# Kernel optimization log

Measured on AMD Instinct MI355X. Metric: run time of the kernel, lower is better.

## Reference

```python
import jax, jax.numpy as jnp
import numpy as np

ACT_DIM = 768
DICT_SIZE = 32768
S0 = 4096          # top-level latent size (dict_size // prod(lower sizes))
S1 = 8             # lower_level_latent_sizes[0]
K = 64             # per-token top-k (applied globally as k * batch)


def setup_inputs() -> dict:
    key = jax.random.key(0)
    ks = jax.random.split(key, 7)
    scale_e = 1.0 / np.sqrt(ACT_DIM)
    scale_d = 1.0 / np.sqrt(DICT_SIZE)
    return {
        "x": jax.random.normal(ks[0], (4096, ACT_DIM), dtype=jnp.float32),
        "W0": jax.random.normal(ks[1], (S0, ACT_DIM), dtype=jnp.float32) * scale_e,
        "b0": jnp.zeros((S0,), dtype=jnp.float32),
        "W1": jax.random.normal(ks[2], (DICT_SIZE, ACT_DIM), dtype=jnp.float32) * scale_e,
        "b1": jnp.zeros((DICT_SIZE,), dtype=jnp.float32),
        "Wd": jax.random.normal(ks[3], (ACT_DIM, DICT_SIZE), dtype=jnp.float32) * scale_d,
        "b_dec": jnp.zeros((ACT_DIM,), dtype=jnp.float32),
    }


def reference(x, W0, b0, W1, b1, Wd, b_dec):
    B = x.shape[0]
    x_centered = x - b_dec                                   # [B, D]
    # hierarchical relu encoders
    l0 = jax.nn.relu(x_centered @ W0.T + b0)                 # [B, S0]
    l1 = jax.nn.relu(x_centered @ W1.T + b1)                 # [B, S0*S1]
    # multiplicative gating: lower-level gate broadcast over finest level
    final_dense = (l1.reshape(B, S0, S1) * l0[:, :, None]).reshape(B, S0 * S1)
    # global batch top-k over flattened [B * dict_size]
    flat = final_dense.reshape(-1)
    k_for_batch = min(K * B, flat.shape[0])
    vals, idx = jax.lax.top_k(flat, k_for_batch)
    sparse_flat = jnp.zeros_like(flat).at[idx].set(vals)
    encoded = sparse_flat.reshape(B, S0 * S1)
    # decode
    x_hat = encoded @ Wd.T + b_dec                           # [B, D]
    return x_hat
```

## Files before the change

### kernel.cpp

```cpp
#include <hip/hip_runtime.h>
#include <stdint.h>

#define DDIM 768
#define BROWS 4096
#define S0N 4096
#define DICT 32768
#define KTOT 262144u
#define PREF 2.0f
#define DELTA 4e-3f
#define CAND_CAP 8388608u
#define BAND_CAP 4096

static constexpr size_t OFF_XH   = 0;
static constexpr size_t OFF_XL   = 6291456;
static constexpr size_t OFF_W0H  = 12582912;
static constexpr size_t OFF_W0L  = 18874368;
static constexpr size_t OFF_W1H  = 25165824;
static constexpr size_t OFF_W1L  = 75497472;
static constexpr size_t OFF_WDT  = 0;
static constexpr size_t OFF_CTRL = 192937984;
static constexpr size_t OFF_ROWC = 193069056;
static constexpr size_t OFF_ROWD = 193085440;
static constexpr size_t OFF_CAND = 201474048;
static constexpr size_t WS_NEED  = 268582912;


typedef __attribute__((ext_vector_type(8))) short bf16x8;
typedef __attribute__((ext_vector_type(4))) float f32x4;

__device__ __forceinline__ unsigned umin_(unsigned a, unsigned b) { return a < b ? a : b; }
__device__ __forceinline__ float relu_(float v) { return v > 0.f ? v : 0.f; }

__device__ __forceinline__ unsigned short f2bf(float f) {
    union { float f; unsigned u; } v; v.f = f;
    unsigned r = v.u + 0x7FFFu + ((v.u >> 16) & 1u);
    return (unsigned short)(r >> 16);
}
__device__ __forceinline__ float bf2f(unsigned short h) {
    union { float f; unsigned u; } v; v.u = ((unsigned)h) << 16;
    return v.f;
}
__device__ __forceinline__ void split1(float a, short& h, short& l) {
    unsigned short hb = f2bf(a);
    float rem = a - bf2f(hb);
    h = (short)hb;
    l = (short)f2bf(rem);
}

__device__ __forceinline__ void gl16(const void* g, void* l) {
    __builtin_amdgcn_global_load_lds(
        (const __attribute__((address_space(1))) void*)g,
        (__attribute__((address_space(3))) void*)l,
        16, 0, 0);
}

__global__ void k_split_x(const float* __restrict__ x, const float* __restrict__ b_dec,
                          short* __restrict__ XH, short* __restrict__ XL) {
    int i = blockIdx.x * 256 + threadIdx.x;
    float4 xv = ((const float4*)x)[i];
    int d = (i % (DDIM / 4)) * 4;
    float4 bv = *(const float4*)(b_dec + d);
    float a[4] = {xv.x - bv.x, xv.y - bv.y, xv.z - bv.z, xv.w - bv.w};
    short4 h, lo;
    split1(a[0], h.x, lo.x); split1(a[1], h.y, lo.y);
    split1(a[2], h.z, lo.z); split1(a[3], h.w, lo.w);
    ((short4*)XH)[i] = h;
    ((short4*)XL)[i] = lo;
}

__global__ void k_split_w(const float* __restrict__ W, short* __restrict__ H,
                          short* __restrict__ L) {
    int i = blockIdx.x * 256 + threadIdx.x;
    float4 wv = ((const float4*)W)[i];
    short4 h, lo;
    split1(wv.x, h.x, lo.x); split1(wv.y, h.y, lo.y);
    split1(wv.z, h.z, lo.z); split1(wv.w, h.w, lo.w);
    ((short4*)H)[i] = h;
    ((short4*)L)[i] = lo;
}

__global__ void k_transpose(const float* __restrict__ Wd, unsigned short* __restrict__ WdT) {
    __shared__ float tile[32][33];
    int j0 = blockIdx.x * 32, d0 = blockIdx.y * 32;
    int tx = threadIdx.x & 31, ty = threadIdx.x >> 5;
#pragma unroll
    for (int i = 0; i < 4; ++i)
        tile[ty + i * 8][tx] = Wd[(size_t)(d0 + ty + i * 8) * DICT + j0 + tx];
    __syncthreads();
#pragma unroll
    for (int i = 0; i < 4; ++i)
        WdT[(size_t)(j0 + ty + i * 8) * DDIM + d0 + tx] = f2bf(tile[tx][ty + i * 8]);
}

__launch_bounds__(512, 2) __global__
void k_mm(const short* __restrict__ XH, const short* __restrict__ XL,
          const short* __restrict__ WH, const short* __restrict__ WL,
          const short* __restrict__ GH, const short* __restrict__ GL,
          const float* __restrict__ bias1, const float* __restrict__ bias0,
          uint2* __restrict__ cand, unsigned* __restrict__ ctrl) {
    __shared__ __align__(16) char smem[139264];

    const int t = threadIdx.x;
    const int w = t >> 6, l = t & 63;
    const int wm = w >> 2, wn = w & 3;
    const int lr = l & 15, lk = l >> 4;

    const int nwg = gridDim.x;
    const int bid = blockIdx.x;
    const int swz = (bid & 7) * (nwg >> 3) + (bid >> 3);
    const int bm = (swz & 15) << 8;
    const int bn = (swz >> 4) << 8;

    const int a0 = 2 * w, a1 = a0 + 1;
    const unsigned aB0 = (unsigned)(bm + (a0 >> 3) * 128 + (a0 & 7) * 16 + lr) * 768u + (unsigned)(lk * 8);
    const unsigned aB1 = (unsigned)(bm + (a1 >> 3) * 128 + (a1 & 7) * 16 + lr) * 768u + (unsigned)(lk * 8);
    const unsigned bB0 = (unsigned)(bn + (a0 >> 2) * 64 + (a0 & 3) * 16 + lr) * 768u + (unsigned)(lk * 8);
    const unsigned bB1 = (unsigned)(bn + (a1 >> 2) * 64 + (a1 & 3) * 16 + lr) * 768u + (unsigned)(lk * 8);
    const unsigned gB0 = (unsigned)((bn >> 3) + w * 16 + lr) * 768u + (unsigned)(lk * 8);
    const int cg0 = (w >> 2) * 8 + (w & 3) * 2;

    f32x4 acc[8][4];
#pragma unroll
    for (int i = 0; i < 8; ++i)
#pragma unroll
        for (int j = 0; j < 4; ++j) acc[i][j] = (f32x4){0.f, 0.f, 0.f, 0.f};
    f32x4 acc_g[2][2];
#pragma unroll
    for (int i = 0; i < 2; ++i)
#pragma unroll
        for (int j = 0; j < 2; ++j) acc_g[i][j] = (f32x4){0.f, 0.f, 0.f, 0.f};

#pragma unroll
    for (int J = 0; J < 3; ++J) {
        const unsigned kb = (unsigned)J * 32u;
        char* dA = smem + J * 16384 + a0 * 1024;
        char* dB = smem + 65536 + J * 16384 + a0 * 1024;
        gl16(XH + aB0 + kb, dA);
        gl16(XH + aB1 + kb, dA + 1024);
        gl16(WH + bB0 + kb, dB);
        gl16(WH + bB1 + kb, dB + 1024);
        if (w < 2) gl16(GH + gB0 + kb, smem + 131072 + J * 2048 + w * 1024);
    }

#pragma unroll 1
    for (int H = 0; H < 72; ++H) {
        if (w < 2) {
            if (H < 70)       asm volatile("s_waitcnt vmcnt(10)" ::: "memory");
            else if (H == 70) asm volatile("s_waitcnt vmcnt(5)" ::: "memory");
            else              asm volatile("s_waitcnt vmcnt(0)" ::: "memory");
        } else {
            if (H < 70)       asm volatile("s_waitcnt vmcnt(8)" ::: "memory");
            else if (H == 70) asm volatile("s_waitcnt vmcnt(4)" ::: "memory");
            else              asm volatile("s_waitcnt vmcnt(0)" ::: "memory");
        }
        __builtin_amdgcn_s_barrier();

        const char* rA = smem + (H & 3) * 16384;
        const char* rB = smem + 65536 + (H & 3) * 16384;
        const char* rG = smem + 131072 + (H & 3) * 2048;

        const int J = H + 3;
        const short* As = XH; const short* Bs = WH; const short* Gs = GH; unsigned kb = 0;
        char* dA = nullptr; char* dB = nullptr; char* dG = nullptr;
        const bool hj = J < 72;
        if (hj) {
            const int ktJ = J >> 1;
            if (ktJ < 12)      { As = XH; Bs = WH; Gs = GH; kb = (unsigned)ktJ * 64u; }
            else if (ktJ < 24) { As = XH; Bs = WL; Gs = GL; kb = (unsigned)(ktJ - 12) * 64u; }
            else               { As = XL; Bs = WH; Gs = GH; kb = (unsigned)(ktJ - 24) * 64u; }
            kb += (unsigned)(J & 1) * 32u;
            dA = smem + (J & 3) * 16384 + a0 * 1024;
            dB = smem + 65536 + (J & 3) * 16384 + a0 * 1024;
            dG = smem + 131072 + (J & 3) * 2048 + w * 1024;
        }

        bf16x8 bfr[4], af[4], bg0, bg1, ag;
#pragma unroll
        for (int nj = 0; nj < 4; ++nj)
            bfr[nj] = *(const bf16x8*)(rB + (wn * 4 + nj) * 1024 + l * 16);
#pragma unroll
        for (int m2 = 0; m2 < 4; ++m2)
            af[m2] = *(const bf16x8*)(rA + (wm * 8 + m2) * 1024 + l * 16);
        bg0 = *(const bf16x8*)(rG + l * 16);
        bg1 = *(const bf16x8*)(rG + 1024 + l * 16);
        ag  = *(const bf16x8*)(rA + cg0 * 1024 + l * 16);
        if (hj) {
            gl16(As + aB0 + kb, dA); gl16(As + aB1 + kb, dA + 1024);
            if (w < 2) gl16(Gs + gB0 + kb, dG);
        }
        __builtin_amdgcn_sched_barrier(0);
        __builtin_amdgcn_s_barrier();
        asm volatile("s_waitcnt lgkmcnt(0)" ::: "memory");
        __builtin_amdgcn_sched_barrier(0);
        __builtin_amdgcn_s_setprio(1);
#pragma unroll
        for (int m2 = 0; m2 < 4; ++m2)
#pragma unroll
            for (int nj = 0; nj < 4; ++nj)
                acc[m2][nj] = __builtin_amdgcn_mfma_f32_16x16x32_bf16(
                    af[m2], bfr[nj], acc[m2][nj], 0, 0, 0);
        acc_g[0][0] = __builtin_amdgcn_mfma_f32_16x16x32_bf16(ag, bg0, acc_g[0][0], 0, 0, 0);
        acc_g[0][1] = __builtin_amdgcn_mfma_f32_16x16x32_bf16(ag, bg1, acc_g[0][1], 0, 0, 0);
        __builtin_amdgcn_s_setprio(0);
        __builtin_amdgcn_s_barrier();

#pragma unroll
        for (int m2 = 0; m2 < 4; ++m2)
            af[m2] = *(const bf16x8*)(rA + (wm * 8 + 4 + m2) * 1024 + l * 16);
        ag = *(const bf16x8*)(rA + (cg0 + 1) * 1024 + l * 16);
        if (hj) { gl16(Bs + bB0 + kb, dB); gl16(Bs + bB1 + kb, dB + 1024); }
        __builtin_amdgcn_sched_barrier(0);
        __builtin_amdgcn_s_barrier();
        asm volatile("s_waitcnt lgkmcnt(0)" ::: "memory");
        __builtin_amdgcn_sched_barrier(0);
        __builtin_amdgcn_s_setprio(1);
#pragma unroll
        for (int m2 = 0; m2 < 4; ++m2)
#pragma unroll
            for (int nj = 0; nj < 4; ++nj)
                acc[4 + m2][nj] = __builtin_amdgcn_mfma_f32_16x16x32_bf16(
                    af[m2], bfr[nj], acc[4 + m2][nj], 0, 0, 0);
        acc_g[1][0] = __builtin_amdgcn_mfma_f32_16x16x32_bf16(ag, bg0, acc_g[1][0], 0, 0, 0);
        acc_g[1][1] = __builtin_amdgcn_mfma_f32_16x16x32_bf16(ag, bg1, acc_g[1][1], 0, 0, 0);
        __builtin_amdgcn_s_setprio(0);
        __builtin_amdgcn_s_barrier();
    }
    __syncthreads();

    float*    gate  = (float*)smem;
    unsigned* pscan = (unsigned*)(smem + 36864);
    const int s0base = bn >> 3;
#pragma unroll
    for (int ri = 0; ri < 2; ++ri)
#pragma unroll
        for (int ci = 0; ci < 2; ++ci)
#pragma unroll
            for (int r = 0; r < 4; ++r) {
                const int grow = w * 32 + ri * 16 + lk * 4 + r;
                const int gcol = ci * 16 + lr;
                gate[grow * 33 + gcol] = relu_(acc_g[ri][ci][r] + bias0[s0base + gcol]);
            }
    __syncthreads();

    unsigned cnt = 0;
#pragma unroll
    for (int mi = 0; mi < 8; ++mi)
#pragma unroll
        for (int nj = 0; nj < 4; ++nj)
#pragma unroll
            for (int r = 0; r < 4; ++r) {
                const int lrow = wm * 128 + mi * 16 + lk * 4 + r;
                const int lcol = wn * 64 + nj * 16 + lr;
                float v = relu_(acc[mi][nj][r] + bias1[bn + lcol]);
                v *= gate[lrow * 33 + (lcol >> 3)];
                acc[mi][nj][r] = v;
                cnt += (v >= PREF) ? 1u : 0u;
            }
    pscan[t] = cnt;
    __syncthreads();
    for (int s = 1; s < 512; s <<= 1) {
        unsigned v2 = (t >= s) ? pscan[t - s] : 0u;
        __syncthreads();
        pscan[t] += v2;
        __syncthreads();
    }
    if (t == 511) pscan[512] = atomicAdd(&ctrl[0], pscan[511]);
    __syncthreads();
    unsigned off = pscan[512] + pscan[t] - cnt;
#pragma unroll
    for (int mi = 0; mi < 8; ++mi)
#pragma unroll
        for (int nj = 0; nj < 4; ++nj)
#pragma unroll
            for (int r = 0; r < 4; ++r) {
                const float v = acc[mi][nj][r];
                if (v >= PREF) {
                    const int row = bm + wm * 128 + mi * 16 + lk * 4 + r;
                    const int col = bn + wn * 64 + nj * 16 + lr;
                    if (off < CAND_CAP)
                        cand[off] = make_uint2(__float_as_uint(v),
                                               ((unsigned)row << 15) | (unsigned)col);
                    ++off;
                }
            }
}

__global__ void k_hist1(const uint2* __restrict__ cand, unsigned* __restrict__ ctrl) {
    __shared__ unsigned h[2048];
    for (int i = threadIdx.x; i < 2048; i += 256) h[i] = 0;
    __syncthreads();
    unsigned n = umin_(ctrl[0], CAND_CAP);
    for (unsigned i = blockIdx.x * 256 + threadIdx.x; i < n; i += gridDim.x * 256)
        atomicAdd(&h[cand[i].x >> 20], 1u);
    __syncthreads();
    unsigned* hist = ctrl + 256;
    for (int i = threadIdx.x; i < 2048; i += 256)
        if (h[i]) atomicAdd(&hist[i], h[i]);
}

__global__ void k_scan1(unsigned* __restrict__ ctrl) {
    __shared__ unsigned hs[2048];
    __shared__ unsigned cs[256];
    const unsigned* h = ctrl + 256;
    int t = threadIdx.x;
    for (int i = t; i < 2048; i += 256) hs[i] = h[i];
    __syncthreads();
    unsigned s = 0;
    for (int b = 0; b < 8; ++b) s += hs[t * 8 + b];
    cs[t] = s;
    __syncthreads();
    if (t == 0) {
        unsigned cum = 0, T = 0, cb = 0;
        for (int c = 255; c >= 0; --c) {
            if (cum + cs[c] >= KTOT) {
                for (int b = c * 8 + 7; b >= c * 8; --b) {
                    cum += hs[b];
                    if (cum >= KTOT) { T = (unsigned)b; cb = cum - hs[b]; break; }
                }
                break;
            }
            cum += cs[c];
        }
        ctrl[1] = T; ctrl[2] = cb;
    }
}

__global__ void k_hist2(const uint2* __restrict__ cand, unsigned* __restrict__ ctrl) {
    unsigned n = umin_(ctrl[0], CAND_CAP);
    unsigned T = ctrl[1];
    unsigned* hist2 = ctrl + 2304;
    for (unsigned i = blockIdx.x * 256 + threadIdx.x; i < n; i += gridDim.x * 256) {
        unsigned u = cand[i].x;
        if ((u >> 20) == T) atomicAdd(&hist2[(u >> 8) & 0xFFFu], 1u);
    }
}

__global__ void k_scan2(unsigned* __restrict__ ctrl) {
    __shared__ unsigned hs[4096];
    __shared__ unsigned cs[256];
    const unsigned* h = ctrl + 2304;
    int t = threadIdx.x;
    for (int i = t; i < 4096; i += 256) hs[i] = h[i];
    __syncthreads();
    unsigned s = 0;
    for (int b = 0; b < 16; ++b) s += hs[t * 16 + b];
    cs[t] = s;
    __syncthreads();
    if (t == 0) {
        unsigned cum = ctrl[2], T2 = 0;
        for (int c = 255; c >= 0; --c) {
            if (cum + cs[c] >= KTOT) {
                for (int b = c * 16 + 15; b >= c * 16; --b) {
                    cum += hs[b];
                    if (cum >= KTOT) { T2 = (unsigned)b; break; }
                }
                break;
            }
            cum += cs[c];
        }
        ctrl[3] = (ctrl[1] << 12) | T2;
    }
}

__global__ void k_band_rows(const uint2* __restrict__ cand, unsigned* __restrict__ ctrl,
                            unsigned* __restrict__ rowc, uint2* __restrict__ rowd) {
    __shared__ unsigned lhi;
    if (threadIdx.x == 0) lhi = 0;
    __syncthreads();
    unsigned n = umin_(ctrl[0], CAND_CAP);
    unsigned H = ctrl[3];
    float lo = __uint_as_float(H << 8) - DELTA;
    float hi = __uint_as_float((H + 1u) << 8) + DELTA;
    unsigned* band_idx = ctrl + 6400;
    unsigned my = 0;
    for (unsigned i = blockIdx.x * 256 + threadIdx.x; i < n; i += gridDim.x * 256) {
        uint2 cv = cand[i];
        float v = __uint_as_float(cv.x);
        if (v > hi) {
            ++my;
            unsigned b = cv.y >> 15;
            unsigned p = atomicAdd(&rowc[b], 1u);
            if (p < 256u) rowd[(b << 8) + p] = make_uint2(cv.y & 32767u, cv.x);
        } else if (v >= lo) {
            unsigned p = atomicAdd(&ctrl[5], 1u);
            if (p < BAND_CAP) band_idx[p] = cv.y;
        }
    }
    atomicAdd(&lhi, my);
    __syncthreads();
    if (threadIdx.x == 0 && lhi) atomicAdd(&ctrl[4], lhi);
}

__global__ void k_f64(const float* __restrict__ x, const float* __restrict__ b_dec,
                      const float* __restrict__ W0, const float* __restrict__ b0,
                      const float* __restrict__ W1, const float* __restrict__ b1,
                      const unsigned* __restrict__ ctrl, double* __restrict__ band_v) {
    unsigned n = umin_(ctrl[5], BAND_CAP);
    unsigned bi = blockIdx.x;
    if (bi >= n) return;
    const unsigned* band_idx = ctrl + 6400;
    unsigned idx = band_idx[bi];
    int b = idx >> 15, j = idx & 32767, s0 = j >> 3;
    int lane = threadIdx.x;
    const float* xr = x + (size_t)b * DDIM;
    const float* w1 = W1 + (size_t)j * DDIM;
    const float* w0 = W0 + (size_t)s0 * DDIM;
    double d1 = 0.0, d0 = 0.0;
    for (int k = lane; k < DDIM; k += 64) {
        double xv = (double)xr[k] - (double)b_dec[k];
        d1 += xv * (double)w1[k];
        d0 += xv * (double)w0[k];
    }
    for (int off = 32; off; off >>= 1) {
        d1 += __shfl_down(d1, off);
        d0 += __shfl_down(d0, off);
    }
    if (lane == 0) {
        double l1v = d1 + (double)b1[j];  l1v = l1v > 0.0 ? l1v : 0.0;
        double l0v = d0 + (double)b0[s0]; l0v = l0v > 0.0 ? l0v : 0.0;
        band_v[bi] = l1v * l0v;
    }
}

__global__ void k_final(unsigned* __restrict__ ctrl, const double* __restrict__ band_v,
                        uint2* __restrict__ extra) {
    __shared__ unsigned long long skey[BAND_CAP];
    __shared__ unsigned sidx[BAND_CAP];
    int t = threadIdx.x;
    unsigned n = umin_(ctrl[5], BAND_CAP);
    unsigned m = 256; while (m < n) m <<= 1;
    const unsigned* band_idx = ctrl + 6400;
    for (unsigned i = t; i < m; i += 256) {
        if (i < n) {
            skey[i] = (unsigned long long)__double_as_longlong(band_v[i]);
            sidx[i] = band_idx[i];
        } else {
            skey[i] = 0ull; sidx[i] = 0xFFFFFFFFu;
        }
    }
    __syncthreads();
    for (unsigned kk = 2; kk <= m; kk <<= 1) {
        for (unsigned jj = kk >> 1; jj > 0; jj >>= 1) {
            for (unsigned i = t; i < m; i += 256) {
                unsigned ixj = i ^ jj;
                if (ixj > i) {
                    unsigned long long ka = skey[i], kb = skey[ixj];
                    unsigned ia = sidx[i], ib = sidx[ixj];
                    bool ab = (ka > kb) || (ka == kb && ia < ib);
                    bool asc = ((i & kk) == 0);
                    if (asc ? !ab : ab) {
                        skey[i] = kb; skey[ixj] = ka;
                        sidx[i] = ib; sidx[ixj] = ia;
                    }
                }
            }
            __syncthreads();
        }
    }
    unsigned c_hi = ctrl[4];
    unsigned k_rem = (c_hi < KTOT) ? (KTOT - c_hi) : 0u;
    if (k_rem > n) k_rem = n;
    if (t == 0) ctrl[6] = k_rem;
    for (unsigned i = t; i < k_rem; i += 256)
        extra[i] = make_uint2(sidx[i],
                              __float_as_uint((float)__longlong_as_double((long long)skey[i])));
}

__global__ void k_rows_b(const unsigned* __restrict__ ctrl, const uint2* __restrict__ extra,
                         unsigned* __restrict__ rowc, uint2* __restrict__ rowd) {
    unsigned k_rem = ctrl[6];
    for (unsigned i = blockIdx.x * 256 + threadIdx.x; i < k_rem; i += gridDim.x * 256) {
        unsigned idx = extra[i].x;
        unsigned b = idx >> 15;
        unsigned p = atomicAdd(&rowc[b], 1u);
        if (p < 256u) rowd[(b << 8) + p] = make_uint2(idx & 32767u, extra[i].y);
    }
}

__launch_bounds__(192) __global__
void k_decode(const uint2* __restrict__ rowd, const unsigned* __restrict__ rowc,
              const unsigned short* __restrict__ WdT, const float* __restrict__ b_dec,
              float* __restrict__ out) {
    __shared__ uint2 e[256];
    int b = blockIdx.x, t = threadIdx.x;
    unsigned c = rowc[b]; if (c > 256u) c = 256u;
    for (int i = t; i < (int)c; i += 192) e[i] = rowd[(b << 8) + i];
    __syncthreads();
    float4 a = *(const float4*)(b_dec + 4 * t);
#pragma unroll 8
    for (unsigned i = 0; i < c; ++i) {
        float v = __uint_as_float(e[i].y);
        ushort4 w4 = *(const ushort4*)(WdT + (size_t)e[i].x * DDIM + 4 * t);
        a.x = fmaf(v, bf2f(w4.x), a.x);
        a.y = fmaf(v, bf2f(w4.y), a.y);
        a.z = fmaf(v, bf2f(w4.z), a.z);
        a.w = fmaf(v, bf2f(w4.w), a.w);
    }
    *(float4*)(out + (size_t)b * DDIM + 4 * t) = a;
}

extern "C" void kernel_launch(void* const* d_in, const int* in_sizes, int n_in,
                              void* d_out, int out_size, void* d_ws, size_t ws_size,
                              hipStream_t stream) {
    const float* x     = (const float*)d_in[0];
    const float* W0    = (const float*)d_in[1];
    const float* b0    = (const float*)d_in[2];
    const float* W1    = (const float*)d_in[3];
    const float* b1    = (const float*)d_in[4];
    const float* Wd    = (const float*)d_in[5];
    const float* b_dec = (const float*)d_in[6];
    float* out = (float*)d_out;

    if (ws_size < WS_NEED) {
        hipMemsetAsync(d_out, 0, (size_t)out_size * sizeof(float), stream);
        return;
    }

    char* ws = (char*)d_ws;
    short*          XH     = (short*)(ws + OFF_XH);
    short*          XL     = (short*)(ws + OFF_XL);
    short*          W0H    = (short*)(ws + OFF_W0H);
    short*          W0L    = (short*)(ws + OFF_W0L);
    short*          W1H    = (short*)(ws + OFF_W1H);
    short*          W1L    = (short*)(ws + OFF_W1L);
    unsigned short* WdT    = (unsigned short*)(ws + OFF_WDT);
    unsigned*       ctrl   = (unsigned*)(ws + OFF_CTRL);
    double*         band_v = (double*)(ws + OFF_CTRL + 65536);
    uint2*          extra  = (uint2*)(ws + OFF_CTRL + 98304);
    unsigned*       rowc   = (unsigned*)(ws + OFF_ROWC);
    uint2*          rowd   = (uint2*)(ws + OFF_ROWD);
    uint2*          cand   = (uint2*)(ws + OFF_CAND);

    hipMemsetAsync(ctrl, 0, 6400 * sizeof(unsigned), stream);
    hipMemsetAsync(rowc, 0, BROWS * sizeof(unsigned), stream);

    k_split_x<<<(BROWS * DDIM / 4) / 256, 256, 0, stream>>>(x, b_dec, XH, XL);
    k_split_w<<<(S0N * DDIM / 4) / 256, 256, 0, stream>>>(W0, W0H, W0L);
    k_split_w<<<(DICT * DDIM / 4) / 256, 256, 0, stream>>>(W1, W1H, W1L);

    k_mm<<<(DICT / 256) * 16, 512, 0, stream>>>(XH, XL, W1H, W1L, W0H, W0L, b1, b0, cand, ctrl);

    k_transpose<<<dim3(DICT / 32, DDIM / 32), 256, 0, stream>>>(Wd, WdT);

    k_hist1<<<1024, 256, 0, stream>>>(cand, ctrl);
    k_scan1<<<1, 256, 0, stream>>>(ctrl);
    k_hist2<<<1024, 256, 0, stream>>>(cand, ctrl);
    k_scan2<<<1, 256, 0, stream>>>(ctrl);
    k_band_rows<<<1024, 256, 0, stream>>>(cand, ctrl, rowc, rowd);
    k_f64<<<BAND_CAP, 64, 0, stream>>>(x, b_dec, W0, b0, W1, b1, ctrl, band_v);
    k_final<<<1, 256, 0, stream>>>(ctrl, band_v, extra);
    k_rows_b<<<32, 256, 0, stream>>>(ctrl, extra, rowc, rowd);

    k_decode<<<BROWS, 192, 0, stream>>>(rowd, rowc, WdT, b_dec, out);
}
```

Measured before the change: 1.133 ms.

## Load A operand directly from global into registers instead of LDS staging

The main encoder GEMM no longer stages the activation (A) tiles through LDS. Each wave now issues direct global dwordx4 loads of its own A fragments (and gate fragments) every iteration, and only the weight tiles keep the LDS multi-buffer. This cuts LDS use roughly in half and merges the two half-iterations into one with fewer barriers. The trade-offs are redundant global/L2 traffic for A across the four wn waves and exposed global-load latency, since A is loaded in the same iteration it is consumed with no prefetch.

```diff
diff --git a/kernel.cpp b/kernel.cpp
--- a/kernel.cpp
+++ b/kernel.cpp
@@ -54,6 +54,12 @@
         16, 0, 0);
 }
 
+__device__ __forceinline__ bf16x8 gload16(const short* p) {
+    bf16x8 r;
+    asm volatile("global_load_dwordx4 %0, %1, off" : "=v"(r) : "v"(p) : "memory");
+    return r;
+}
+
 __global__ void k_split_x(const float* __restrict__ x, const float* __restrict__ b_dec,
                           short* __restrict__ XH, short* __restrict__ XL) {
     int i = blockIdx.x * 256 + threadIdx.x;
@@ -98,7 +104,7 @@
           const short* __restrict__ GH, const short* __restrict__ GL,
           const float* __restrict__ bias1, const float* __restrict__ bias0,
           uint2* __restrict__ cand, unsigned* __restrict__ ctrl) {
-    __shared__ __align__(16) char smem[139264];
+    __shared__ __align__(16) char smem[73728];
 
     const int t = threadIdx.x;
     const int w = t >> 6, l = t & 63;
@@ -112,12 +118,16 @@
     const int bn = (swz >> 4) << 8;
 
     const int a0 = 2 * w, a1 = a0 + 1;
-    const unsigned aB0 = (unsigned)(bm + (a0 >> 3) * 128 + (a0 & 7) * 16 + lr) * 768u + (unsigned)(lk * 8);
-    const unsigned aB1 = (unsigned)(bm + (a1 >> 3) * 128 + (a1 & 7) * 16 + lr) * 768u + (unsigned)(lk * 8);
     const unsigned bB0 = (unsigned)(bn + (a0 >> 2) * 64 + (a0 & 3) * 16 + lr) * 768u + (unsigned)(lk * 8);
     const unsigned bB1 = (unsigned)(bn + (a1 >> 2) * 64 + (a1 & 3) * 16 + lr) * 768u + (unsigned)(lk * 8);
     const unsigned gB0 = (unsigned)((bn >> 3) + w * 16 + lr) * 768u + (unsigned)(lk * 8);
-    const int cg0 = (w >> 2) * 8 + (w & 3) * 2;
+
+    unsigned aOff[8];
+#pragma unroll
+    for (int mi = 0; mi < 8; ++mi)
+        aOff[mi] = (unsigned)(bm + (wm * 8 + mi) * 16 + lr) * 768u + (unsigned)(lk * 8);
+    const unsigned gOff0 = (unsigned)(bm + w * 32 + lr) * 768u + (unsigned)(lk * 8);
+    const unsigned gOff1 = gOff0 + 16u * 768u;
 
     f32x4 acc[8][4];
 #pragma unroll
@@ -133,97 +143,72 @@
 #pragma unroll
     for (int J = 0; J < 3; ++J) {
         const unsigned kb = (unsigned)J * 32u;
-        char* dA = smem + J * 16384 + a0 * 1024;
-        char* dB = smem + 65536 + J * 16384 + a0 * 1024;
-        gl16(XH + aB0 + kb, dA);
-        gl16(XH + aB1 + kb, dA + 1024);
+        char* dB = smem + J * 16384 + a0 * 1024;
         gl16(WH + bB0 + kb, dB);
         gl16(WH + bB1 + kb, dB + 1024);
-        if (w < 2) gl16(GH + gB0 + kb, smem + 131072 + J * 2048 + w * 1024);
+        if (w < 2) gl16(GH + gB0 + kb, smem + 65536 + J * 2048 + w * 1024);
     }
 
 #pragma unroll 1
     for (int H = 0; H < 72; ++H) {
-        if (w < 2) {
-            if (H < 70)       asm volatile("s_waitcnt vmcnt(10)" ::: "memory");
-            else if (H == 70) asm volatile("s_waitcnt vmcnt(5)" ::: "memory");
-            else              asm volatile("s_waitcnt vmcnt(0)" ::: "memory");
+        __builtin_amdgcn_s_barrier();
+
+        const short* Ax; unsigned kbA;
+        if (H < 24)      { Ax = XH; kbA = (unsigned)H * 32u; }
+        else if (H < 48) { Ax = XH; kbA = (unsigned)(H - 24) * 32u; }
+        else             { Ax = XL; kbA = (unsigned)(H - 48) * 32u; }
+
+        bf16x8 afn[8], agn0, agn1;
+#pragma unroll
+        for (int mi = 0; mi < 8; ++mi)
+            afn[mi] = gload16(Ax + aOff[mi] + kbA);
+        agn0 = gload16(Ax + gOff0 + kbA);
+        agn1 = gload16(Ax + gOff1 + kbA);
+
+        const int J = H + 3;
+        if (J < 72) {
+            const short* Bs; const short* Gs; unsigned kb;
+            const int ktJ = J >> 1;
+            if (ktJ < 12)      { Bs = WH; Gs = GH; kb = (unsigned)ktJ * 64u; }
+            else if (ktJ < 24) { Bs = WL; Gs = GL; kb = (unsigned)(ktJ - 12) * 64u; }
+            else               { Bs = WH; Gs = GH; kb = (unsigned)(ktJ - 24) * 64u; }
+            kb += (unsigned)(J & 1) * 32u;
+            char* dB = smem + (J & 3) * 16384 + a0 * 1024;
+            gl16(Bs + bB0 + kb, dB);
+            gl16(Bs + bB1 + kb, dB + 1024);
+            if (w < 2) gl16(Gs + gB0 + kb, smem + 65536 + (J & 3) * 2048 + w * 1024);
+        }
+
+        if (H < 69) {
+            if (w < 2) asm volatile("s_waitcnt vmcnt(3)" ::: "memory");
+            else       asm volatile("s_waitcnt vmcnt(2)" ::: "memory");
         } else {
-            if (H < 70)       asm volatile("s_waitcnt vmcnt(8)" ::: "memory");
-            else if (H == 70) asm volatile("s_waitcnt vmcnt(4)" ::: "memory");
-            else              asm volatile("s_waitcnt vmcnt(0)" ::: "memory");
-        }
-        __builtin_amdgcn_s_barrier();
-
-        const char* rA = smem + (H & 3) * 16384;
-        const char* rB = smem + 65536 + (H & 3) * 16384;
-        const char* rG = smem + 131072 + (H & 3) * 2048;
-
-        const int J = H + 3;
-        const short* As = XH; const short* Bs = WH; const short* Gs = GH; unsigned kb = 0;
-        char* dA = nullptr; char* dB = nullptr; char* dG = nullptr;
-        const bool hj = J < 72;
-        if (hj) {
-            const int ktJ = J >> 1;
-            if (ktJ < 12)      { As = XH; Bs = WH; Gs = GH; kb = (unsigned)ktJ * 64u; }
-            else if (ktJ < 24) { As = XH; Bs = WL; Gs = GL; kb = (unsigned)(ktJ - 12) * 64u; }
-            else               { As = XL; Bs = WH; Gs = GH; kb = (unsigned)(ktJ - 24) * 64u; }
-            kb += (unsigned)(J & 1) * 32u;
-            dA = smem + (J & 3) * 16384 + a0 * 1024;
-            dB = smem + 65536 + (J & 3) * 16384 + a0 * 1024;
-            dG = smem + 131072 + (J & 3) * 2048 + w * 1024;
-        }
-
-        bf16x8 bfr[4], af[4], bg0, bg1, ag;
+            asm volatile("s_waitcnt vmcnt(0)" ::: "memory");
+        }
+        __builtin_amdgcn_sched_barrier(0);
+
+        const char* rB = smem + (H & 3) * 16384;
+        const char* rG = smem + 65536 + (H & 3) * 2048;
+        bf16x8 bfr[4];
 #pragma unroll
         for (int nj = 0; nj < 4; ++nj)
             bfr[nj] = *(const bf16x8*)(rB + (wn * 4 + nj) * 1024 + l * 16);
-#pragma unroll
-        for (int m2 = 0; m2 < 4; ++m2)
-            af[m2] = *(const bf16x8*)(rA + (wm * 8 + m2) * 1024 + l * 16);
-        bg0 = *(const bf16x8*)(rG + l * 16);
-        bg1 = *(const bf16x8*)(rG + 1024 + l * 16);
-        ag  = *(const bf16x8*)(rA + cg0 * 1024 + l * 16);
-        if (hj) {
-            gl16(As + aB0 + kb, dA); gl16(As + aB1 + kb, dA + 1024);
-            if (w < 2) gl16(Gs + gB0 + kb, dG);
-        }
-        __builtin_amdgcn_sched_barrier(0);
-        __builtin_amdgcn_s_barrier();
+        bf16x8 bg0 = *(const bf16x8*)(rG + l * 16);
+        bf16x8 bg1 = *(const bf16x8*)(rG + 1024 + l * 16);
+
+        __builtin_amdgcn_s_setprio(1);
+#pragma unroll
+        for (int mi = 0; mi < 8; ++mi)
+#pragma unroll
+            for (int nj = 0; nj < 4; ++nj)
+                acc[mi][nj] = __builtin_amdgcn_mfma_f32_16x16x32_bf16(
+                    afn[mi], bfr[nj], acc[mi][nj], 0, 0, 0);
+        acc_g[0][0] = __builtin_amdgcn_mfma_f32_16x16x32_bf16(agn0, bg0, acc_g[0][0], 0, 0, 0);
+        acc_g[0][1] = __builtin_amdgcn_mfma_f32_16x16x32_bf16(agn0, bg1, acc_g[0][1], 0, 0, 0);
+        acc_g[1][0] = __builtin_amdgcn_mfma_f32_16x16x32_bf16(agn1, bg0, acc_g[1][0], 0, 0, 0);
+        acc_g[1][1] = __builtin_amdgcn_mfma_f32_16x16x32_bf16(agn1, bg1, acc_g[1][1], 0, 0, 0);
+        __builtin_amdgcn_s_setprio(0);
         asm volatile("s_waitcnt lgkmcnt(0)" ::: "memory");
-        __builtin_amdgcn_sched_barrier(0);
-        __builtin_amdgcn_s_setprio(1);
-#pragma unroll
-        for (int m2 = 0; m2 < 4; ++m2)
-#pragma unroll
-            for (int nj = 0; nj < 4; ++nj)
-                acc[m2][nj] = __builtin_amdgcn_mfma_f32_16x16x32_bf16(
-                    af[m2], bfr[nj], acc[m2][nj], 0, 0, 0);
-        acc_g[0][0] = __builtin_amdgcn_mfma_f32_16x16x32_bf16(ag, bg0, acc_g[0][0], 0, 0, 0);
-        acc_g[0][1] = __builtin_amdgcn_mfma_f32_16x16x32_bf16(ag, bg1, acc_g[0][1], 0, 0, 0);
-        __builtin_amdgcn_s_setprio(0);
-        __builtin_amdgcn_s_barrier();
-
-#pragma unroll
-        for (int m2 = 0; m2 < 4; ++m2)
-            af[m2] = *(const bf16x8*)(rA + (wm * 8 + 4 + m2) * 1024 + l * 16);
-        ag = *(const bf16x8*)(rA + (cg0 + 1) * 1024 + l * 16);
-        if (hj) { gl16(Bs + bB0 + kb, dB); gl16(Bs + bB1 + kb, dB + 1024); }
-        __builtin_amdgcn_sched_barrier(0);
-        __builtin_amdgcn_s_barrier();
-        asm volatile("s_waitcnt lgkmcnt(0)" ::: "memory");
-        __builtin_amdgcn_sched_barrier(0);
-        __builtin_amdgcn_s_setprio(1);
-#pragma unroll
-        for (int m2 = 0; m2 < 4; ++m2)
-#pragma unroll
-            for (int nj = 0; nj < 4; ++nj)
-                acc[4 + m2][nj] = __builtin_amdgcn_mfma_f32_16x16x32_bf16(
-                    af[m2], bfr[nj], acc[4 + m2][nj], 0, 0, 0);
-        acc_g[1][0] = __builtin_amdgcn_mfma_f32_16x16x32_bf16(ag, bg0, acc_g[1][0], 0, 0, 0);
-        acc_g[1][1] = __builtin_amdgcn_mfma_f32_16x16x32_bf16(ag, bg1, acc_g[1][1], 0, 0, 0);
-        __builtin_amdgcn_s_setprio(0);
-        __builtin_amdgcn_s_barrier();
     }
     __syncthreads();
 
```

Measured after the change: 2.241 ms. 97.8% more time.
